# Optimization experiments

Hardware: AMD Instinct MI355X
Metric: run time of the kernel (lower is better)

## Reference

```python
import jax, jax.numpy as jnp
import numpy as np
import math

# B queries, N complex ambient dim, M codebook entries, S payload dim, K quad nodes
B, N, M, S, K = 1024, 128, 8192, 256, 8
EPS_TOTAL = 1e-3
OVERLAP, ANISO = 0.25, 0.75
_t, _w = np.polynomial.hermite.hermgauss(K)
GH_T = jnp.asarray(_t, jnp.float32)
GH_W = jnp.asarray(_w, jnp.float32)


def _init_sigmas():
    # mirrors CPSFFusedCodebook._init_sigmas (log-space for numerical safety at N=128)
    rho = 1.0 + ANISO
    logV = (N / 2.0) * math.log(math.pi) - math.lgamma(N / 2.0 + 1.0)
    log_r = (math.log(OVERLAP) - math.log(M) - logV - math.log(rho)) / N
    r_perp = math.exp(log_r)
    s_perp = 2.0 * math.pi * r_perp ** 2
    return rho * rho * s_perp, s_perp


def setup_inputs() -> dict:
    key = jax.random.key(0)
    ks = jax.random.split(key, 12)
    u = lambda k, sh: jax.random.uniform(k, sh, jnp.float32, -1.0, 1.0)
    s_par, s_perp = _init_sigmas()
    return {
        "z_re": u(ks[0], (B, N)), "z_im": u(ks[1], (B, N)),
        "d_re": u(ks[2], (B, N)), "d_im": u(ks[3], (B, N)),
        "zj_re": 0.5 * u(ks[4], (M, N)), "zj_im": 0.5 * u(ks[5], (M, N)),
        "dj_re": 0.5 * u(ks[6], (M, N)), "dj_im": 0.5 * u(ks[7], (M, N)),
        "T_re": u(ks[8], (M, S)), "T_im": u(ks[9], (M, S)),
        "alpha": jax.random.uniform(ks[10], (M,), jnp.float32, 0.5, 1.5),
        "sigma_par": jnp.full((M,), s_par, jnp.float32),
        "sigma_perp": jnp.full((M,), s_perp, jnp.float32),
    }


def _unit(xr, xi):
    n = jnp.sqrt(jnp.sum(xr * xr + xi * xi, -1, keepdims=True))
    n = jnp.where(n == 0, jnp.ones_like(n), n)
    return xr / n, xi / n


def _forward(z_re, z_im, d_re, d_im, zj_re, zj_im, dj_re, dj_im,
             T_re, T_im, alpha, sigma_par, sigma_perp):
    tiny = jnp.float32(np.finfo(np.float32).tiny)
    dur, dui = _unit(d_re, d_im)          # autonorm_vec_d
    djr, dji = _unit(dj_re, dj_im)        # autonorm_vec_d_j
    a = jnp.maximum(alpha, tiny)
    sp = jnp.maximum(sigma_par, tiny)
    sq = jnp.maximum(sigma_perp, tiny)

    # proj[b,m] = <d_j, z - z_j> (conj-linear in d_j); all via GEMMs, no [B,M,N] tensor
    pr = z_re @ djr.T + z_im @ dji.T - jnp.sum(djr * zj_re + dji * zj_im, -1)[None, :]
    pi = z_im @ djr.T - z_re @ dji.T - jnp.sum(djr * zj_im - dji * zj_re, -1)[None, :]

    # |z - z_j|^2 via GEMM expansion
    dz2 = (jnp.sum(z_re * z_re + z_im * z_im, -1)[:, None]
           + jnp.sum(zj_re * zj_re + zj_im * zj_im, -1)[None, :]
           - 2.0 * (z_re @ zj_re.T + z_im @ zj_im.T))
    perp2 = jnp.maximum(dz2 - (pr * pr + pi * pi), 0.0)  # component orthogonal to d_j

    # Gauss-Hermite quadrature along the codebook direction, scaled per-code
    scale = jnp.sqrt(sp / jnp.pi)                     # [M]
    t = GH_T[None, :] * scale[:, None]                # [M,K] quad offsets
    par2 = (pr[:, :, None] - t[None]) ** 2 + (pi * pi)[:, :, None]   # [B,M,K]
    env = jnp.exp(-jnp.pi * (par2 / sp[None, :, None]
                             + (perp2 / sq[None, :])[:, :, None]))
    rho = jnp.einsum('bmk,k->bm', env, GH_W) * (scale / jnp.sqrt(jnp.pi))[None, :]

    # angular alignment |<d_j, d>|^2
    ar = dur @ djr.T + dui @ dji.T
    ai = dui @ djr.T - dur @ dji.T
    align = ar * ar + ai * ai

    w = a[None, :] * align * rho                      # [B,M] real mixture weights
    den = jnp.sum(w, -1) + EPS_TOTAL                  # [B]
    out_re = (w @ T_re) / den[:, None]                # [B,S]
    out_im = (w @ T_im) / den[:, None]
    return jnp.stack([out_re, out_im], -1)            # [B,S,2] == complex [B,S]


def reference(z_re, z_im, d_re, d_im, zj_re, zj_im, dj_re, dj_im,
              T_re, T_im, alpha, sigma_par, sigma_perp):
    return _forward(z_re, z_im, d_re, d_im, zj_re, zj_im, dj_re, dj_im,
                    T_re, T_im, alpha, sigma_par, sigma_perp)
```

## Files before the change

kernel.cpp:

```cpp
#include <hip/hip_runtime.h>
#include <math.h>

#define Bq 1024
#define Nn 128
#define Mm 8192
#define Ss 256

typedef _Float16 f16;
typedef _Float16 f16x8 __attribute__((ext_vector_type(8)));
typedef _Float16 f16x4 __attribute__((ext_vector_type(4)));
typedef float f32x4 __attribute__((ext_vector_type(4)));

#define PI_F 3.14159265358979323846f
#define INV_SQRT_PI 0.5641895835477563f
#define TINY_F 1.17549435e-38f
#define EPS_TOTAL 1e-3f
#define WSC 1024.0f

#define GLOAD16(g, l) \
    __builtin_amdgcn_global_load_lds((const __attribute__((address_space(1))) void*)(g), \
                                     (__attribute__((address_space(3))) void*)(l), 16, 0, 0)

__global__ void cpsf_prep_pack(
    const float* __restrict__ z_re, const float* __restrict__ z_im,
    const float* __restrict__ d_re, const float* __restrict__ d_im,
    const float* __restrict__ zj_re, const float* __restrict__ zj_im,
    const float* __restrict__ dj_re, const float* __restrict__ dj_im,
    const float* __restrict__ T_re, const float* __restrict__ T_im,
    const float* __restrict__ alpha, const float* __restrict__ sp_,
    const float* __restrict__ sq_, float* __restrict__ z2,
    float* __restrict__ cm, f16* __restrict__ Az, f16* __restrict__ Bp,
    f16* __restrict__ Tt, int Mc, int m0g, int n0, int n1, int n2, int mshift)
{
    __shared__ float tsm[2 * 64 * 65];
    const int bx = blockIdx.x;
    const int tid = threadIdx.x;
    const int wid = tid >> 6;
    const int l = tid & 63;

    if (bx < n0) {
        const int b = bx * 4 + wid;
        const int o = b * Nn;
        float dr0 = d_re[o + l], dr1 = d_re[o + l + 64];
        float di0 = d_im[o + l], di1 = d_im[o + l + 64];
        float zr0 = z_re[o + l], zr1 = z_re[o + l + 64];
        float zi0 = z_im[o + l], zi1 = z_im[o + l + 64];
        float sd = dr0*dr0 + di0*di0 + dr1*dr1 + di1*di1;
        float sz = zr0*zr0 + zi0*zi0 + zr1*zr1 + zi1*zi1;
#pragma unroll
        for (int off = 1; off < 64; off <<= 1) {
            sd += __shfl_xor(sd, off);
            sz += __shfl_xor(sz, off);
        }
        float nd = sqrtf(sd);
        nd = (nd == 0.0f) ? 1.0f : nd;
        float inv = 1.0f / nd;
        if (l == 0) z2[b] = sz;
        int map = l >> 5, c = l & 31;
        int k8 = (c & 15) * 8;
        const float* src = (map == 0) ? ((c < 16) ? z_re : z_im)
                                      : ((c < 16) ? d_re : d_im);
        float s = (map == 0) ? 1.0f : inv;
        float4 v0 = *(const float4*)(src + (size_t)b * Nn + k8);
        float4 v1 = *(const float4*)(src + (size_t)b * Nn + k8 + 4);
        f16x8 ov = {(f16)(v0.x*s), (f16)(v0.y*s), (f16)(v0.z*s), (f16)(v0.w*s),
                    (f16)(v1.x*s), (f16)(v1.y*s), (f16)(v1.z*s), (f16)(v1.w*s)};
        *(f16x8*)(Az + ((size_t)l * 1024 + b) * 8) = ov;
    } else if (bx < n0 + n1) {
        const int m = (bx - n0) * 4 + wid;
        const int o = m * Nn;
        float dr0 = dj_re[o + l], dr1 = dj_re[o + l + 64];
        float di0 = dj_im[o + l], di1 = dj_im[o + l + 64];
        float zr0 = zj_re[o + l], zr1 = zj_re[o + l + 64];
        float zi0 = zj_im[o + l], zi1 = zj_im[o + l + 64];
        float snd = dr0*dr0 + di0*di0 + dr1*dr1 + di1*di1;
        float sc1 = dr0*zr0 + di0*zi0 + dr1*zr1 + di1*zi1;
        float sc2 = dr0*zi0 - di0*zr0 + dr1*zi1 - di1*zr1;
        float sz2 = zr0*zr0 + zi0*zi0 + zr1*zr1 + zi1*zi1;
#pragma unroll
        for (int off = 1; off < 64; off <<= 1) {
            snd += __shfl_xor(snd, off);
            sc1 += __shfl_xor(sc1, off);
            sc2 += __shfl_xor(sc2, off);
            sz2 += __shfl_xor(sz2, off);
        }
        if (l == 0) {
            float nd = sqrtf(snd);
            nd = (nd == 0.0f) ? 1.0f : nd;
            float inv = 1.0f / nd;
            cm[0*Mm + m] = inv;
            cm[1*Mm + m] = sc1 * inv;
            cm[2*Mm + m] = sc2 * inv;
            cm[3*Mm + m] = sz2;
            float sp = fmaxf(sp_[m], TINY_F);
            float sq = fmaxf(sq_[m], TINY_F);
            float sc = sqrtf(sp / PI_F);
            cm[4*Mm + m] = PI_F / sp;
            cm[5*Mm + m] = PI_F / sq;
            cm[6*Mm + m] = fmaxf(alpha[m], TINY_F) * sc * INV_SQRT_PI;
            cm[7*Mm + m] = sc;
        }
    } else if (bx < n0 + n1 + n2) {
        int idx = (bx - n0 - n1) * 256 + tid;
        int m = idx & (Mc - 1);
        int pc = idx >> mshift;
        int p = pc >> 5, c = pc & 31;
        int mg = m0g + m;
        int hi = (c >= 16);
        int k8 = (c & 15) * 8;
        const float* src;
        float sgn = 1.0f;
        if (p == 0)      src = hi ? dj_im : dj_re;
        else if (p == 1) { src = hi ? dj_re : dj_im; sgn = hi ? 1.0f : -1.0f; }
        else             src = hi ? zj_im : zj_re;
        float4 v0 = *(const float4*)(src + (size_t)mg * Nn + k8);
        float4 v1 = *(const float4*)(src + (size_t)mg * Nn + k8 + 4);
        f16x8 o = {(f16)(v0.x*sgn), (f16)(v0.y*sgn), (f16)(v0.z*sgn), (f16)(v0.w*sgn),
                   (f16)(v1.x*sgn), (f16)(v1.y*sgn), (f16)(v1.z*sgn), (f16)(v1.w*sgn)};
        *(f16x8*)(Bp + (size_t)idx * 8) = o;
    } else {
        const int bt = bx - n0 - n1 - n2;
        const int nmb = Mc >> 6;
        const int mb = (bt & (nmb - 1)) * 64, sb = (bt / nmb) * 64;
        float* tr = tsm;
        float* ti = tsm + 64 * 65;
        const int i0 = tid >> 6, jj0 = tid & 63;
#pragma unroll
        for (int it = 0; it < 16; ++it) {
            int i = it * 4 + i0;
            tr[i * 65 + jj0] = T_re[(size_t)(m0g + mb + i) * Ss + sb + jj0];
            ti[i * 65 + jj0] = T_im[(size_t)(m0g + mb + i) * Ss + sb + jj0];
        }
        __syncthreads();
#pragma unroll
        for (int it = 0; it < 16; ++it) {
            int jj = it * 4 + i0;
            int sp = (sb + jj) * 2;
            Tt[(size_t)sp * Mc + mb + jj0]       = (f16)tr[jj0 * 65 + jj];
            Tt[(size_t)(sp + 1) * Mc + mb + jj0] = (f16)ti[jj0 * 65 + jj];
        }
    }
}

__global__ __launch_bounds__(256, 3) void cpsf_gemm_w(
    const f16* __restrict__ Az, const f16* __restrict__ Bp,
    const float* __restrict__ cm, const float* __restrict__ z2v,
    f16* __restrict__ wbuf, float* __restrict__ den, int Mc, int m0g)
{
    __shared__ __align__(16) f16 sm[2 * 1280 * 8];
    const int tid = threadIdx.x;
    const int wid = tid >> 6;
    const int lane = tid & 63;
    const int q = lane >> 4;
    const int li = lane & 15;

    const int nmt = gridDim.x;
    const int sbid = blockIdx.x + nmt * blockIdx.y;
    const int xcd = sbid & 7;
    const int jb = sbid >> 3;
    const int mpg = nmt >> 3;
    const int mtile = xcd * mpg + (jb & (mpg - 1));
    const int btile = jb / mpg;
    const int mb0 = mtile * 64;
    const int bb0 = btile * 64;
    const int wb0 = (wid >> 1) * 32;
    const int wm0 = (wid & 1) * 32;
    const int BUFO = 1280 * 8;

    const f16* gp[5];
    size_t gstep[5];
    f16* lb[5];
#pragma unroll
    for (int i = 0; i < 5; ++i) {
        const f16* src;
        size_t st;
        if (i == 0) {
            src = Az + ((size_t)wid * 1024 + bb0 + lane) * 8;
            st = (size_t)4 * 1024 * 8;
        } else if (i == 1) {
            src = Az + ((size_t)(32 + wid) * 1024 + bb0 + lane) * 8;
            st = (size_t)4 * 1024 * 8;
        } else {
            int j = (i - 2) * 4 + wid;
            int g = j / 3, p = j % 3;
            src = Bp + ((size_t)(p * 32 + g) * Mc + mb0 + lane) * 8;
            st = (size_t)4 * Mc * 8;
        }
        gp[i] = src; gstep[i] = st;
        lb[i] = sm + (size_t)(i * 256 + wid * 64) * 8;
    }

    f32x4 accP[2][2][3];
    f32x4 accQ[2][2][2];
#pragma unroll
    for (int t = 0; t < 2; ++t)
#pragma unroll
        for (int u = 0; u < 2; ++u) {
#pragma unroll
            for (int p = 0; p < 3; ++p) accP[t][u][p] = (f32x4){0.f,0.f,0.f,0.f};
#pragma unroll
            for (int p = 0; p < 2; ++p) accQ[t][u][p] = (f32x4){0.f,0.f,0.f,0.f};
        }

#pragma unroll
    for (int i = 0; i < 5; ++i) { GLOAD16(gp[i], lb[i]); gp[i] += gstep[i]; }

#pragma unroll
    for (int ks = 0; ks < 8; ++ks) {
        const int p = ks & 1;
        if (ks > 0) {
            __builtin_amdgcn_sched_barrier(0);
            __builtin_amdgcn_s_barrier();
        }
        if (ks < 7) {
#pragma unroll
            for (int i = 0; i < 5; ++i) { GLOAD16(gp[i], lb[i] + (p ^ 1) * BUFO); gp[i] += gstep[i]; }
            asm volatile("s_waitcnt vmcnt(5)" ::: "memory");
        } else {
            asm volatile("s_waitcnt vmcnt(0)" ::: "memory");
        }
        __builtin_amdgcn_sched_barrier(0);
        __builtin_amdgcn_s_barrier();

        const f16* bs = sm + p * BUFO;
        f16x8 az[2], au[2], bf[3][2];
#pragma unroll
        for (int t = 0; t < 2; ++t) {
            az[t] = *(const f16x8*)(bs + (size_t)(q * 64 + wb0 + t * 16 + li) * 8);
            au[t] = *(const f16x8*)(bs + (size_t)(256 + q * 64 + wb0 + t * 16 + li) * 8);
        }
#pragma unroll
        for (int pp = 0; pp < 3; ++pp)
#pragma unroll
            for (int u = 0; u < 2; ++u)
                bf[pp][u] = *(const f16x8*)(bs + (size_t)(512 + q * 192 + pp * 64 + wm0 + u * 16 + li) * 8);

        __builtin_amdgcn_s_setprio(1);
#pragma unroll
        for (int t = 0; t < 2; ++t)
#pragma unroll
            for (int u = 0; u < 2; ++u) {
#pragma unroll
                for (int pp = 0; pp < 3; ++pp)
                    accP[t][u][pp] = __builtin_amdgcn_mfma_f32_16x16x32_f16(az[t], bf[pp][u], accP[t][u][pp], 0, 0, 0);
#pragma unroll
                for (int pp = 0; pp < 2; ++pp)
                    accQ[t][u][pp] = __builtin_amdgcn_mfma_f32_16x16x32_f16(au[t], bf[pp][u], accQ[t][u][pp], 0, 0, 0);
            }
        __builtin_amdgcn_s_setprio(0);
    }

    const float GT[8] = {-2.9306374202572440f, -1.9816567566958429f,
                         -1.1571937124467802f, -0.3811869902073221f,
                          0.3811869902073221f,  1.1571937124467802f,
                          1.9816567566958429f,  2.9306374202572440f};
    const float GW[8] = {1.9960407221136762e-04f, 1.7077983007413475e-02f,
                         2.0780232581489188e-01f, 6.6114701255824129e-01f,
                         6.6114701255824129e-01f, 2.0780232581489188e-01f,
                         1.7077983007413475e-02f, 1.9960407221136762e-04f};

    float iv[2], c1[2], c2[2], zj2[2], isp[2], isq[2], cf[2], scl[2];
#pragma unroll
    for (int u = 0; u < 2; ++u) {
        int mg = m0g + mb0 + wm0 + u * 16 + li;
        iv[u]  = cm[0*Mm + mg];
        c1[u]  = cm[1*Mm + mg];  c2[u]  = cm[2*Mm + mg];
        zj2[u] = cm[3*Mm + mg];  isp[u] = cm[4*Mm + mg];
        isq[u] = cm[5*Mm + mg];  cf[u]  = cm[6*Mm + mg];
        scl[u] = cm[7*Mm + mg];
    }

    float dsum[2][4];
#pragma unroll
    for (int t = 0; t < 2; ++t)
#pragma unroll
        for (int r = 0; r < 4; ++r) dsum[t][r] = 0.f;

#pragma unroll
    for (int t = 0; t < 2; ++t) {
#pragma unroll
        for (int r = 0; r < 4; ++r) {
            const int b = bb0 + wb0 + t * 16 + q * 4 + r;
            const float z2b = z2v[b];
#pragma unroll
            for (int u = 0; u < 2; ++u) {
                float pr = accP[t][u][0][r] * iv[u] - c1[u];
                float pi = accP[t][u][1][r] * iv[u] - c2[u];
                float dz2 = z2b + zj2[u] - 2.0f * accP[t][u][2][r];
                float perp2 = fmaxf(dz2 - pr * pr - pi * pi, 0.0f);
                float base = -(isq[u] * perp2 + isp[u] * pi * pi);
                float rho = 0.0f;
#pragma unroll
                for (int k = 0; k < 8; ++k) {
                    float dd = pr - scl[u] * GT[k];
                    rho = fmaf(GW[k], __expf(base - isp[u] * dd * dd), rho);
                }
                float ar = accQ[t][u][0][r] * iv[u], ai = accQ[t][u][1][r] * iv[u];
                float wv = cf[u] * (ar * ar + ai * ai) * rho;
                dsum[t][r] += wv;
                wbuf[(size_t)b * Mc + mb0 + wm0 + u * 16 + li] = (f16)(wv * WSC);
            }
        }
    }
#pragma unroll
    for (int t = 0; t < 2; ++t)
#pragma unroll
        for (int r = 0; r < 4; ++r) {
            float v = dsum[t][r];
            v += __shfl_xor(v, 1);
            v += __shfl_xor(v, 2);
            v += __shfl_xor(v, 4);
            v += __shfl_xor(v, 8);
            if (li == 0) atomicAdd(den + bb0 + wb0 + t * 16 + q * 4 + r, v);
        }
}

__global__ __launch_bounds__(256, 2) void cpsf_gemm_out(
    const f16* __restrict__ wbuf, const f16* __restrict__ Tt,
    float* __restrict__ osl, int Mc, int Kw, int zs)
{
    __shared__ __align__(16) f16 sm[2 * 2048 * 8];
    const int tid = threadIdx.x;
    const int wid = tid >> 6;
    const int lane = tid & 63;
    const int q = lane >> 4;
    const int li = lane & 15;

    const int bid = blockIdx.x;
    const int xcd = bid & 7;
    const int j = bid >> 3;
    const int s = j / zs;
    const int g = xcd * zs + (j % zs);
    const int zb = g >> 3;
    const int yb = g & 7;
    const int sb0 = s * 128;
    const int bb0 = yb * 128;
    const int kz0 = zb * Kw;
    float* oz = osl + (size_t)zb * ((size_t)Bq * 512);
    const int wb0 = (wid >> 1) * 64;
    const int ws0 = (wid & 1) * 64;
    const int BUFO = 2048 * 8;

    const f16* gp[8];
    f16* lb[8];
#pragma unroll
    for (int i = 0; i < 8; ++i) {
        int c = i * 4 + wid;
        const f16* src;
        if (c < 16) {
            int gch = c >> 1, row = (c & 1) * 64 + lane;
            src = wbuf + (size_t)(bb0 + row) * Mc + kz0 + gch * 8;
        } else {
            int c2 = c - 16;
            int gch = c2 >> 1, row = (c2 & 1) * 64 + lane;
            src = Tt + (size_t)(sb0 + row) * Mc + kz0 + gch * 8;
        }
        gp[i] = src;
        lb[i] = sm + (size_t)(c * 64) * 8;
    }

    f32x4 acc[4][4];
#pragma unroll
    for (int t = 0; t < 4; ++t)
#pragma unroll
        for (int u = 0; u < 4; ++u) acc[t][u] = (f32x4){0.f,0.f,0.f,0.f};

#pragma unroll
    for (int i = 0; i < 8; ++i) { GLOAD16(gp[i], lb[i]); gp[i] += 64; }

    const int nk = Kw >> 6;
    for (int kc = 0; kc < nk; ++kc) {
        const int p = kc & 1;
        if (kc > 0) {
            __builtin_amdgcn_sched_barrier(0);
            __builtin_amdgcn_s_barrier();
        }
        if (kc + 1 < nk) {
#pragma unroll
            for (int i = 0; i < 8; ++i) { GLOAD16(gp[i], lb[i] + (p ^ 1) * BUFO); gp[i] += 64; }
            asm volatile("s_waitcnt vmcnt(8)" ::: "memory");
        } else {
            asm volatile("s_waitcnt vmcnt(0)" ::: "memory");
        }
        __builtin_amdgcn_sched_barrier(0);
        __builtin_amdgcn_s_barrier();

        const f16* bs = sm + p * BUFO;
#pragma unroll
        for (int kk = 0; kk < 2; ++kk) {
            f16x8 af[4], bf[4];
#pragma unroll
            for (int t = 0; t < 4; ++t)
                af[t] = *(const f16x8*)(bs + (size_t)((kk * 4 + q) * 128 + wb0 + t * 16 + li) * 8);
#pragma unroll
            for (int u = 0; u < 4; ++u)
                bf[u] = *(const f16x8*)(bs + (size_t)(1024 + (kk * 4 + q) * 128 + ws0 + u * 16 + li) * 8);
            __builtin_amdgcn_s_setprio(1);
#pragma unroll
            for (int t = 0; t < 4; ++t)
#pragma unroll
                for (int u = 0; u < 4; ++u)
                    acc[t][u] = __builtin_amdgcn_mfma_f32_16x16x32_f16(af[t], bf[u], acc[t][u], 0, 0, 0);
            __builtin_amdgcn_s_setprio(0);
        }
    }
#pragma unroll
    for (int t = 0; t < 4; ++t)
#pragma unroll
        for (int u = 0; u < 4; ++u)
#pragma unroll
            for (int r = 0; r < 4; ++r)
                oz[(size_t)(bb0 + wb0 + t * 16 + q * 4 + r) * 512 + sb0 + ws0 + u * 16 + li] =
                    acc[t][u][r];
}

__global__ void cpsf_fin(const float* __restrict__ osl, const float* __restrict__ den,
                         float* __restrict__ out, int Z)
{
    int i = (blockIdx.x * 256 + threadIdx.x) * 4;
    float4 s = {0.f, 0.f, 0.f, 0.f};
    for (int z = 0; z < Z; ++z) {
        float4 v = *(const float4*)(osl + (size_t)z * ((size_t)Bq * 512) + i);
        s.x += v.x; s.y += v.y; s.z += v.z; s.w += v.w;
    }
    float d = 1.0f / ((den[i >> 9] + EPS_TOTAL) * WSC);
    float4 o = {s.x * d, s.y * d, s.z * d, s.w * d};
    *(float4*)(out + i) = o;
}

extern "C" void kernel_launch(void* const* d_in, const int* in_sizes, int n_in,
                              void* d_out, int out_size, void* d_ws, size_t ws_size,
                              hipStream_t stream)
{
    (void)in_sizes; (void)n_in; (void)out_size;
    const float* z_re  = (const float*)d_in[0];
    const float* z_im  = (const float*)d_in[1];
    const float* d_re  = (const float*)d_in[2];
    const float* d_im  = (const float*)d_in[3];
    const float* zj_re = (const float*)d_in[4];
    const float* zj_im = (const float*)d_in[5];
    const float* dj_re = (const float*)d_in[6];
    const float* dj_im = (const float*)d_in[7];
    const float* T_re  = (const float*)d_in[8];
    const float* T_im  = (const float*)d_in[9];
    const float* alpha = (const float*)d_in[10];
    const float* s_par = (const float*)d_in[11];
    const float* s_perp= (const float*)d_in[12];

    const size_t SL = (size_t)Bq * 512 * 4;
    const size_t fixedA = 4096 + 4096 + (size_t)8 * Mm * 4 + (size_t)Bq * 512 * 2;

    int Mc = 0, Z = 0;
    const int Zopt[3] = {16, 8, 4};
    const int Mopt[4] = {8192, 4096, 2048, 1024};
    for (int zi = 0; zi < 3 && !Mc; ++zi)
        for (int mi = 0; mi < 4; ++mi) {
            int Zc = Zopt[zi], Mcc = Mopt[mi];
            int nch = Mm / Mcc;
            if (Zc % nch) continue;
            int Kwc = Mcc / (Zc / nch);
            if (Kwc < 64 || (Kwc & 63)) continue;
            size_t need = (size_t)Zc * SL + fixedA + (size_t)4608 * Mcc;
            if (need <= ws_size) { Mc = Mcc; Z = Zc; break; }
        }
    if (!Mc) { Mc = 1024; Z = 8; }
    const int nch = Mm / Mc;
    const int zs = Z / nch;
    const int Kw = Mc / zs;
    const int mshift = 31 - __builtin_clz((unsigned)Mc);

    char* w8 = (char*)d_ws;
    const size_t o_sl  = 0;
    const size_t o_den = o_sl + (size_t)Z * SL;
    const size_t o_z2  = o_den + 4096;
    const size_t o_cm  = o_z2 + 4096;
    const size_t o_az  = o_cm + (size_t)8 * Mm * 4;
    const size_t o_ch  = o_az + (size_t)Bq * 512 * 2;

    float* osl = (float*)(w8 + o_sl);
    float* den = (float*)(w8 + o_den);
    float* z2  = (float*)(w8 + o_z2);
    float* cm  = (float*)(w8 + o_cm);
    f16*   Az  = (f16*)(w8 + o_az);
    f16*   Bp  = (f16*)(w8 + o_ch);
    f16*   Tt  = (f16*)(w8 + o_ch + (size_t)1536 * Mc);
    f16*   wb  = (f16*)(w8 + o_ch + (size_t)2560 * Mc);

    hipMemsetAsync(w8 + o_den, 0, 4096, stream);

    for (int ci = 0; ci < nch; ++ci) {
        const int m0 = ci * Mc;
        const int n0 = (ci == 0) ? 256 : 0;
        const int n1 = (ci == 0) ? Mm / 4 : 0;
        const int n2 = (96 * Mc) / 256;
        const int n3 = (Mc / 64) * (Ss / 64);
        cpsf_prep_pack<<<n0 + n1 + n2 + n3, 256, 0, stream>>>(
            z_re, z_im, d_re, d_im, zj_re, zj_im, dj_re, dj_im, T_re, T_im,
            alpha, s_par, s_perp, z2, cm, Az, Bp, Tt, Mc, m0, n0, n1, n2, mshift);
        cpsf_gemm_w<<<dim3(Mc / 64, Bq / 64), 256, 0, stream>>>(
            Az, Bp, cm, z2, wb, den, Mc, m0);
        cpsf_gemm_out<<<32 * zs, 256, 0, stream>>>(
            wb, Tt, osl + (size_t)ci * zs * ((size_t)Bq * 512), Mc, Kw, zs);
    }
    cpsf_fin<<<(Bq * 512) / 1024, 256, 0, stream>>>(osl, den, (float*)d_out, Z);
}
```

Before: 213.8 us.

## Derive rotated dj operand in-register and triple-buffer the W GEMM LDS pipeline

Stops packing the third, sign-flipped dj plane in the prep kernel. The GEMM rebuilds it from the stored dj plane by swapping re/im halves through a q^2 LDS read and flipping sign bits with an XOR mask. This cuts the B-operand global traffic and the packed buffer size by a third. The main loop also moves from double to triple buffering in LDS, keeping two k-steps of loads in flight, which adds LDS footprint and carries a risk in the new buffer indexing and waitcnt counts.

Measured after the change: 216.5 us. Within noise of the previous version (+1.2%).

```diff
diff --git a/kernel.cpp b/kernel.cpp
--- a/kernel.cpp
+++ b/kernel.cpp
@@ -108,15 +108,12 @@
         int mg = m0g + m;
         int hi = (c >= 16);
         int k8 = (c & 15) * 8;
-        const float* src;
-        float sgn = 1.0f;
-        if (p == 0)      src = hi ? dj_im : dj_re;
-        else if (p == 1) { src = hi ? dj_re : dj_im; sgn = hi ? 1.0f : -1.0f; }
-        else             src = hi ? zj_im : zj_re;
+        const float* src = (p == 0) ? (hi ? dj_im : dj_re)
+                                    : (hi ? zj_im : zj_re);
         float4 v0 = *(const float4*)(src + (size_t)mg * Nn + k8);
         float4 v1 = *(const float4*)(src + (size_t)mg * Nn + k8 + 4);
-        f16x8 o = {(f16)(v0.x*sgn), (f16)(v0.y*sgn), (f16)(v0.z*sgn), (f16)(v0.w*sgn),
-                   (f16)(v1.x*sgn), (f16)(v1.y*sgn), (f16)(v1.z*sgn), (f16)(v1.w*sgn)};
+        f16x8 o = {(f16)v0.x, (f16)v0.y, (f16)v0.z, (f16)v0.w,
+                   (f16)v1.x, (f16)v1.y, (f16)v1.z, (f16)v1.w};
         *(f16x8*)(Bp + (size_t)idx * 8) = o;
     } else {
         const int bt = bx - n0 - n1 - n2;
@@ -147,7 +144,7 @@
     const float* __restrict__ cm, const float* __restrict__ z2v,
     f16* __restrict__ wbuf, float* __restrict__ den, int Mc, int m0g)
 {
-    __shared__ __align__(16) f16 sm[2 * 1280 * 8];
+    __shared__ __align__(16) f16 sm[3 * 1024 * 8];
     const int tid = threadIdx.x;
     const int wid = tid >> 6;
     const int lane = tid & 63;
@@ -165,27 +162,20 @@
     const int bb0 = btile * 64;
     const int wb0 = (wid >> 1) * 32;
     const int wm0 = (wid & 1) * 32;
-    const int BUFO = 1280 * 8;
-
-    const f16* gp[5];
-    size_t gstep[5];
-    f16* lb[5];
-#pragma unroll
-    for (int i = 0; i < 5; ++i) {
+    const int BUFO = 1024 * 8;
+
+    const int cw = (wid < 2) ? wid : (14 + wid);
+    const f16* gp[4];
+    size_t gstep[4];
+    f16* lb[4];
+#pragma unroll
+    for (int i = 0; i < 4; ++i) {
         const f16* src;
         size_t st;
-        if (i == 0) {
-            src = Az + ((size_t)wid * 1024 + bb0 + lane) * 8;
-            st = (size_t)4 * 1024 * 8;
-        } else if (i == 1) {
-            src = Az + ((size_t)(32 + wid) * 1024 + bb0 + lane) * 8;
-            st = (size_t)4 * 1024 * 8;
-        } else {
-            int j = (i - 2) * 4 + wid;
-            int g = j / 3, p = j % 3;
-            src = Bp + ((size_t)(p * 32 + g) * Mc + mb0 + lane) * 8;
-            st = (size_t)4 * Mc * 8;
-        }
+        if (i == 0)      { src = Az + ((size_t)cw * 1024 + bb0 + lane) * 8;        st = (size_t)2 * 1024 * 8; }
+        else if (i == 1) { src = Az + ((size_t)(32 + cw) * 1024 + bb0 + lane) * 8; st = (size_t)2 * 1024 * 8; }
+        else if (i == 2) { src = Bp + ((size_t)cw * Mc + mb0 + lane) * 8;          st = (size_t)2 * Mc * 8; }
+        else             { src = Bp + ((size_t)(32 + cw) * Mc + mb0 + lane) * 8;   st = (size_t)2 * Mc * 8; }
         gp[i] = src; gstep[i] = st;
         lb[i] = sm + (size_t)(i * 256 + wid * 64) * 8;
     }
@@ -202,50 +192,59 @@
             for (int p = 0; p < 2; ++p) accQ[t][u][p] = (f32x4){0.f,0.f,0.f,0.f};
         }
 
-#pragma unroll
-    for (int i = 0; i < 5; ++i) { GLOAD16(gp[i], lb[i]); gp[i] += gstep[i]; }
+    const unsigned smask = (q < 2) ? 0x80008000u : 0u;
+
+#pragma unroll
+    for (int i = 0; i < 4; ++i) { GLOAD16(gp[i], lb[i]); gp[i] += gstep[i]; }
+#pragma unroll
+    for (int i = 0; i < 4; ++i) { GLOAD16(gp[i], lb[i] + BUFO); gp[i] += gstep[i]; }
 
 #pragma unroll
     for (int ks = 0; ks < 8; ++ks) {
-        const int p = ks & 1;
+        const int pb = ks % 3;
         if (ks > 0) {
             __builtin_amdgcn_sched_barrier(0);
             __builtin_amdgcn_s_barrier();
         }
-        if (ks < 7) {
-#pragma unroll
-            for (int i = 0; i < 5; ++i) { GLOAD16(gp[i], lb[i] + (p ^ 1) * BUFO); gp[i] += gstep[i]; }
-            asm volatile("s_waitcnt vmcnt(5)" ::: "memory");
+        if (ks < 6) {
+#pragma unroll
+            for (int i = 0; i < 4; ++i) { GLOAD16(gp[i], lb[i] + ((ks + 2) % 3) * BUFO); gp[i] += gstep[i]; }
+            asm volatile("s_waitcnt vmcnt(8)" ::: "memory");
+        } else if (ks == 6) {
+            asm volatile("s_waitcnt vmcnt(4)" ::: "memory");
         } else {
             asm volatile("s_waitcnt vmcnt(0)" ::: "memory");
         }
         __builtin_amdgcn_sched_barrier(0);
         __builtin_amdgcn_s_barrier();
 
-        const f16* bs = sm + p * BUFO;
-        f16x8 az[2], au[2], bf[3][2];
+        const f16* bs = sm + pb * BUFO;
+        f16x8 az[2], au[2], bfd[2], bfz[2], bf1[2];
 #pragma unroll
         for (int t = 0; t < 2; ++t) {
             az[t] = *(const f16x8*)(bs + (size_t)(q * 64 + wb0 + t * 16 + li) * 8);
             au[t] = *(const f16x8*)(bs + (size_t)(256 + q * 64 + wb0 + t * 16 + li) * 8);
         }
 #pragma unroll
-        for (int pp = 0; pp < 3; ++pp)
-#pragma unroll
-            for (int u = 0; u < 2; ++u)
-                bf[pp][u] = *(const f16x8*)(bs + (size_t)(512 + q * 192 + pp * 64 + wm0 + u * 16 + li) * 8);
+        for (int u = 0; u < 2; ++u) {
+            bfd[u] = *(const f16x8*)(bs + (size_t)(512 + q * 64 + wm0 + u * 16 + li) * 8);
+            bfz[u] = *(const f16x8*)(bs + (size_t)(768 + q * 64 + wm0 + u * 16 + li) * 8);
+            f16x8 r = *(const f16x8*)(bs + (size_t)(512 + (q ^ 2) * 64 + wm0 + u * 16 + li) * 8);
+            int4 vi = *(int4*)&r;
+            vi.x ^= smask; vi.y ^= smask; vi.z ^= smask; vi.w ^= smask;
+            bf1[u] = *(f16x8*)&vi;
+        }
 
         __builtin_amdgcn_s_setprio(1);
 #pragma unroll
         for (int t = 0; t < 2; ++t)
 #pragma unroll
             for (int u = 0; u < 2; ++u) {
-#pragma unroll
-                for (int pp = 0; pp < 3; ++pp)
-                    accP[t][u][pp] = __builtin_amdgcn_mfma_f32_16x16x32_f16(az[t], bf[pp][u], accP[t][u][pp], 0, 0, 0);
-#pragma unroll
-                for (int pp = 0; pp < 2; ++pp)
-                    accQ[t][u][pp] = __builtin_amdgcn_mfma_f32_16x16x32_f16(au[t], bf[pp][u], accQ[t][u][pp], 0, 0, 0);
+                accP[t][u][0] = __builtin_amdgcn_mfma_f32_16x16x32_f16(az[t], bfd[u], accP[t][u][0], 0, 0, 0);
+                accP[t][u][1] = __builtin_amdgcn_mfma_f32_16x16x32_f16(az[t], bf1[u], accP[t][u][1], 0, 0, 0);
+                accP[t][u][2] = __builtin_amdgcn_mfma_f32_16x16x32_f16(az[t], bfz[u], accP[t][u][2], 0, 0, 0);
+                accQ[t][u][0] = __builtin_amdgcn_mfma_f32_16x16x32_f16(au[t], bfd[u], accQ[t][u][0], 0, 0, 0);
+                accQ[t][u][1] = __builtin_amdgcn_mfma_f32_16x16x32_f16(au[t], bf1[u], accQ[t][u][1], 0, 0, 0);
             }
         __builtin_amdgcn_s_setprio(0);
     }
@@ -460,7 +459,7 @@
             if (Zc % nch) continue;
             int Kwc = Mcc / (Zc / nch);
             if (Kwc < 64 || (Kwc & 63)) continue;
-            size_t need = (size_t)Zc * SL + fixedA + (size_t)4608 * Mcc;
+            size_t need = (size_t)Zc * SL + fixedA + (size_t)4096 * Mcc;
             if (need <= ws_size) { Mc = Mcc; Z = Zc; break; }
         }
     if (!Mc) { Mc = 1024; Z = 8; }
@@ -483,8 +482,8 @@
     float* cm  = (float*)(w8 + o_cm);
     f16*   Az  = (f16*)(w8 + o_az);
     f16*   Bp  = (f16*)(w8 + o_ch);
-    f16*   Tt  = (f16*)(w8 + o_ch + (size_t)1536 * Mc);
-    f16*   wb  = (f16*)(w8 + o_ch + (size_t)2560 * Mc);
+    f16*   Tt  = (f16*)(w8 + o_ch + (size_t)1024 * Mc);
+    f16*   wb  = (f16*)(w8 + o_ch + (size_t)2048 * Mc);
 
     hipMemsetAsync(w8 + o_den, 0, 4096, stream);
 
@@ -492,7 +491,7 @@
         const int m0 = ci * Mc;
         const int n0 = (ci == 0) ? 256 : 0;
         const int n1 = (ci == 0) ? Mm / 4 : 0;
-        const int n2 = (96 * Mc) / 256;
+        const int n2 = (64 * Mc) / 256;
         const int n3 = (Mc / 64) * (Ss / 64);
         cpsf_prep_pack<<<n0 + n1 + n2 + n3, 256, 0, stream>>>(
             z_re, z_im, d_re, d_im, zj_re, zj_im, dj_re, dj_im, T_re, T_im,
```
